# Kernel tuning notes

Measured on AMD Instinct MI355X. Metric: run time of the kernel, lower is better.

Reference implementation:

```python
import jax, jax.numpy as jnp
import numpy as np

B, H, S, D = 1, 8, 4096, 64
NSPAN, SPAN_LEN = 8, 512  # 8 contiguous spans of 512 tokens
RADIUS_SQ = 6.25          # default radius=2.5 squared (current_radius_sq buffer)


def setup_inputs() -> dict:
    key = jax.random.key(0)
    kq, kk, kv = jax.random.split(key, 3)
    q = jax.random.normal(kq, (B, H, S, D), jnp.float32)
    k = jax.random.normal(kk, (B, H, S, D), jnp.float32)
    v = jax.random.normal(kv, (B, H, S, D), jnp.float32)
    # span topology, as produced by update_buffers(spans)
    span_ids = jnp.repeat(jnp.arange(NSPAN, dtype=jnp.int32), SPAN_LEN)  # [S]
    causal_per_span = jnp.array([(i % 2) == 0 for i in range(NSPAN)])     # alternate causal/spatial
    is_causal = causal_per_span[span_ids]                                 # [S] bool
    # non-causal spans carry a 16x32 spatial grid (per _generate_grid); causal spans have coords 0
    gy, gx = jnp.meshgrid(jnp.arange(16, dtype=jnp.float32),
                          jnp.arange(32, dtype=jnp.float32), indexing='ij')
    grid = jnp.stack([gy, gx], axis=-1).reshape(SPAN_LEN, 2)
    coords = jnp.where(is_causal[:, None], 0.0, jnp.tile(grid, (NSPAN, 1)))  # [S,2]
    return {"q": q, "k": k, "v": v, "coords": coords,
            "span_ids": span_ids, "is_causal": is_causal}


def _mask(coords, span_ids, is_causal):
    # mask_mod from get_mask, vectorized over (q_idx, kv_idx) -> [S,S] bool
    qs = span_ids[:, None]
    ks = span_ids[None, :]
    is_history = qs > ks
    is_same = qs == ks
    idx = jnp.arange(span_ids.shape[0])
    valid_time = (~is_causal[:, None]) | (idx[:, None] >= idx[None, :])
    dist_sq = jnp.sum((coords[:, None, :] - coords[None, :, :]) ** 2, axis=-1)
    valid_space = dist_sq < RADIUS_SQ
    return is_history | (is_same & valid_time & valid_space)


def reference(q, k, v, coords, span_ids, is_causal):
    mask = _mask(coords, span_ids, is_causal)                       # [S,S]
    scale = 1.0 / jnp.sqrt(jnp.float32(D))
    scores = jnp.einsum('bhqd,bhkd->bhqk', q, k) * scale            # [B,H,S,S]
    scores = jnp.where(mask, scores, jnp.float32(-1e30))
    attn = jax.nn.softmax(scores, axis=-1)
    return jnp.einsum('bhqk,bhkd->bhqd', attn, v)                   # [B,H,S,D]
```

## Files before the change

### kernel.cpp

```cpp
#include <hip/hip_runtime.h>

#define S_LEN 4096
#define DH 64
#define SPAN 512
#define FIXED_M 8.0f

typedef _Float16 f16x8 __attribute__((ext_vector_type(8)));
typedef __fp16 fp16v2 __attribute__((ext_vector_type(2)));
typedef float f32x4 __attribute__((ext_vector_type(4)));

#define MFMA16 __builtin_amdgcn_mfma_f32_16x16x32_f16

__device__ __forceinline__ f16x8 load_cvt8(const float* __restrict__ p) {
  float4 a = *(const float4*)p;
  float4 b = *(const float4*)(p + 4);
  f16x8 r;
  r[0] = (_Float16)a.x; r[1] = (_Float16)a.y; r[2] = (_Float16)a.z; r[3] = (_Float16)a.w;
  r[4] = (_Float16)b.x; r[5] = (_Float16)b.y; r[6] = (_Float16)b.z; r[7] = (_Float16)b.w;
  return r;
}

__global__ __launch_bounds__(256) void prep_frag(const float* __restrict__ k,
                                                 const float* __restrict__ v,
                                                 _Float16* __restrict__ KF,
                                                 _Float16* __restrict__ VF) {
  const int b = blockIdx.x;
  const int h = b >> 7, tile = b & 127;
  const int kv0 = tile * 32;
  __shared__ _Float16 LK[32][64];
  __shared__ _Float16 LV[64][36];
  const int t = threadIdx.x;
  const int row = t >> 3, cb = (t & 7) * 8;
  {
    const float* kp = k + ((size_t)h * S_LEN + kv0 + row) * DH + cb;
    float4 a = *(const float4*)kp;
    float4 bq = *(const float4*)(kp + 4);
    LK[row][cb + 0] = (_Float16)a.x;  LK[row][cb + 1] = (_Float16)a.y;
    LK[row][cb + 2] = (_Float16)a.z;  LK[row][cb + 3] = (_Float16)a.w;
    LK[row][cb + 4] = (_Float16)bq.x; LK[row][cb + 5] = (_Float16)bq.y;
    LK[row][cb + 6] = (_Float16)bq.z; LK[row][cb + 7] = (_Float16)bq.w;
  }
  {
    const float* vp = v + ((size_t)h * S_LEN + kv0 + row) * DH + cb;
    float4 a = *(const float4*)vp;
    float4 bq = *(const float4*)(vp + 4);
    LV[cb + 0][row] = (_Float16)a.x;  LV[cb + 1][row] = (_Float16)a.y;
    LV[cb + 2][row] = (_Float16)a.z;  LV[cb + 3][row] = (_Float16)a.w;
    LV[cb + 4][row] = (_Float16)bq.x; LV[cb + 5][row] = (_Float16)bq.y;
    LV[cb + 6][row] = (_Float16)bq.z; LV[cb + 7][row] = (_Float16)bq.w;
  }
  __syncthreads();
  const int l = t & 63, c = l & 15, g = l >> 4;
  const size_t tb = (size_t)(h * 128 + tile) * 2048;
  {
    const int ch = t >> 6;
    f16x8 r = *(const f16x8*)&LK[16 * (ch >> 1) + c][32 * (ch & 1) + 8 * g];
    *(f16x8*)(KF + tb + (size_t)(ch * 64 + l) * 8) = r;
  }
  {
    const int dd = t >> 6;
    f16x8 r;
    #pragma unroll
    for (int jj = 0; jj < 4; ++jj) {
      r[jj]     = LV[16 * dd + c][4 * g + jj];
      r[4 + jj] = LV[16 * dd + c][16 + 4 * g + jj];
    }
    *(f16x8*)(VF + tb + (size_t)(dd * 64 + l) * 8) = r;
  }
}

template<int MODE>
__device__ __forceinline__ void kv_tile(
    const _Float16* __restrict__ kbase, const _Float16* __restrict__ vbase,
    int kt, int q_base, int c, int g,
    const f16x8 (&qf)[2][2], float (&l_run)[2], f32x4 (&of)[2][4])
{
  const int toff = (kt >> 5) * 2048;
  f16x8 kf0a = *(const f16x8*)(kbase + toff);
  f16x8 kf0b = *(const f16x8*)(kbase + toff + 512);
  f16x8 kf1a = *(const f16x8*)(kbase + toff + 1024);
  f16x8 kf1b = *(const f16x8*)(kbase + toff + 1536);
  f16x8 vf0  = *(const f16x8*)(vbase + toff);
  f16x8 vf1  = *(const f16x8*)(vbase + toff + 512);
  f16x8 vf2  = *(const f16x8*)(vbase + toff + 1024);
  f16x8 vf3  = *(const f16x8*)(vbase + toff + 1536);

  const float SCL = 0.18033688011112042f;

  #pragma unroll
  for (int grp = 0; grp < 2; ++grp) {
    f32x4 st0 = {0.f, 0.f, 0.f, 0.f};
    f32x4 st1 = {0.f, 0.f, 0.f, 0.f};
    st0 = MFMA16(kf0a, qf[grp][0], st0, 0, 0, 0);
    st0 = MFMA16(kf0b, qf[grp][1], st0, 0, 0, 0);
    st1 = MFMA16(kf1a, qf[grp][0], st1, 0, 0, 0);
    st1 = MFMA16(kf1b, qf[grp][1], st1, 0, 0, 0);

    const int qg = q_base + 16 * grp + c;
    float p[8];
    #pragma unroll
    for (int t = 0; t < 2; ++t) {
      #pragma unroll
      for (int r = 0; r < 4; ++r) {
        float pe = __builtin_amdgcn_exp2f(fmaf(t ? st1[r] : st0[r], SCL, -FIXED_M));
        if (MODE == 1) {
          int kvi = kt + 16 * t + 4 * g + r;
          pe = (kvi <= qg) ? pe : 0.f;
        } else if (MODE == 2) {
          int kvi = kt + 16 * t + 4 * g + r;
          int pq = qg & (SPAN - 1), pk = kvi & (SPAN - 1);
          int dy = (pq >> 5) - (pk >> 5);
          int dx = (pq & 31) - (pk & 31);
          pe = (dy * dy + dx * dx <= 6) ? pe : 0.f;
        }
        p[4 * t + r] = pe;
      }
    }
    l_run[grp] += ((p[0] + p[1]) + (p[2] + p[3])) + ((p[4] + p[5]) + (p[6] + p[7]));

    union { unsigned int w[4]; f16x8 v; } u;
    union { fp16v2 h; unsigned int w; } t0, t1, t2, t3;
    t0.h = __builtin_amdgcn_cvt_pkrtz(p[0], p[1]);
    t1.h = __builtin_amdgcn_cvt_pkrtz(p[2], p[3]);
    t2.h = __builtin_amdgcn_cvt_pkrtz(p[4], p[5]);
    t3.h = __builtin_amdgcn_cvt_pkrtz(p[6], p[7]);
    u.w[0] = t0.w; u.w[1] = t1.w; u.w[2] = t2.w; u.w[3] = t3.w;
    f16x8 pa = u.v;

    of[grp][0] = MFMA16(vf0, pa, of[grp][0], 0, 0, 0);
    of[grp][1] = MFMA16(vf1, pa, of[grp][1], 0, 0, 0);
    of[grp][2] = MFMA16(vf2, pa, of[grp][2], 0, 0, 0);
    of[grp][3] = MFMA16(vf3, pa, of[grp][3], 0, 0, 0);
  }
}

__global__ __launch_bounds__(256) void msa_attn13(
    const float* __restrict__ q, const _Float16* __restrict__ KF,
    const _Float16* __restrict__ VF, float* __restrict__ PO,
    float* __restrict__ PL)
{
  const int tid = threadIdx.x;
  const int lane = tid & 63, w = tid >> 6;
  const int c = lane & 15, g = lane >> 4;

  const int b = blockIdx.x;
  const int h = b & 7;
  const int unit = (b >> 3) * 4 + w;

  int s, sub, slot, klo, khi, mode;
  {
    int r = unit;
    if (r < 448) {
      s = 1;
      while (r >= 16 * s) { r -= 16 * s; ++s; }
      sub = r & 15;
      slot = r >> 4;
      klo = slot << 9;
      khi = klo + 512;
      mode = 0;
    } else {
      r -= 448;
      s = r >> 4; sub = r & 15;
      slot = s;
      const int hist_end = s * SPAN;
      const int q_base = s * SPAN + sub * 32;
      if ((s & 1) == 0) {
        klo = hist_end; khi = q_base + 32; mode = 1;
      } else {
        klo = q_base - 96; if (klo < hist_end) klo = hist_end;
        khi = q_base + 128;
        const int s1 = hist_end + SPAN; if (khi > s1) khi = s1;
        mode = 2;
      }
    }
  }
  const int q_base = s * SPAN + sub * 32;

  const float* Qh = q + (size_t)h * S_LEN * DH;
  const _Float16* kbase = KF + (size_t)h * 262144 + (size_t)lane * 8;
  const _Float16* vbase = VF + (size_t)h * 262144 + (size_t)lane * 8;

  f16x8 qf[2][2];
  #pragma unroll
  for (int grp = 0; grp < 2; ++grp) {
    const float* qp = Qh + (size_t)(q_base + 16 * grp + c) * DH + 8 * g;
    qf[grp][0] = load_cvt8(qp);
    qf[grp][1] = load_cvt8(qp + 32);
  }

  float l_run[2] = {0.f, 0.f};
  f32x4 of[2][4];
  #pragma unroll
  for (int a = 0; a < 2; ++a)
    #pragma unroll
    for (int bb = 0; bb < 4; ++bb) of[a][bb] = (f32x4){0.f, 0.f, 0.f, 0.f};

  if (mode == 0) {
    for (int kt = klo; kt < khi; kt += 32)
      kv_tile<0>(kbase, vbase, kt, q_base, c, g, qf, l_run, of);
  } else if (mode == 1) {
    for (int kt = klo; kt < khi; kt += 32)
      kv_tile<1>(kbase, vbase, kt, q_base, c, g, qf, l_run, of);
  } else {
    for (int kt = klo; kt < khi; kt += 32)
      kv_tile<2>(kbase, vbase, kt, q_base, c, g, qf, l_run, of);
  }

  #pragma unroll
  for (int grp = 0; grp < 2; ++grp) {
    l_run[grp] += __shfl_xor(l_run[grp], 16);
    l_run[grp] += __shfl_xor(l_run[grp], 32);
  }

  const size_t sl_idx = (size_t)(h * 128 + s * 16 + sub) * 8 + slot;
  float* po = PO + sl_idx * 2048;
  float* pl = PL + sl_idx * 32;
  if (g == 0) { pl[c] = l_run[0]; pl[16 + c] = l_run[1]; }
  #pragma unroll
  for (int grp = 0; grp < 2; ++grp)
    #pragma unroll
    for (int dd = 0; dd < 4; ++dd)
      *(f32x4*)(po + (16 * grp + c) * 64 + 16 * dd + 4 * g) = of[grp][dd];
}

__global__ __launch_bounds__(256) void finalize13(const float* __restrict__ PO,
                                                  const float* __restrict__ PL,
                                                  float* __restrict__ out) {
  const int strip = blockIdx.x;
  const int h = strip >> 7, idx = strip & 127;
  const int s = idx >> 4, sub = idx & 15;
  const int t = threadIdx.x;
  const int row = t >> 3, colb = (t & 7) * 8;
  const float* po = PO + (size_t)strip * 8 * 2048 + row * 64 + colb;
  const float* pl = PL + (size_t)strip * 8 * 32 + row;
  f32x4 a0 = {0.f, 0.f, 0.f, 0.f}, a1 = {0.f, 0.f, 0.f, 0.f};
  float l = 0.f;
  for (int sl = 0; sl <= s; ++sl) {
    a0 += *(const f32x4*)(po + sl * 2048);
    a1 += *(const f32x4*)(po + sl * 2048 + 4);
    l  += pl[sl * 32];
  }
  const float inv = 1.0f / l;
  f32x4 o0, o1;
  #pragma unroll
  for (int j = 0; j < 4; ++j) { o0[j] = a0[j] * inv; o1[j] = a1[j] * inv; }
  const int orow = s * SPAN + sub * 32 + row;
  float* op = out + ((size_t)h * S_LEN + orow) * DH + colb;
  *(f32x4*)op = o0;
  *(f32x4*)(op + 4) = o1;
}

__global__ __launch_bounds__(256, 3) void msa_attn10(
    const float* __restrict__ q, const _Float16* __restrict__ KF,
    const _Float16* __restrict__ VF, float* __restrict__ out)
{
  const int tid = threadIdx.x;
  const int lane = tid & 63, w = tid >> 6;
  const int c = lane & 15, g = lane >> 4;

  const int i = blockIdx.x;
  const int h = i & 7;
  const int m = i >> 3;
  const int jj = m >> 5;
  const int sidx = ((m & 7) + jj) & 7;
  const int span = (sidx & 1) ? 7 - (sidx >> 1) : (sidx >> 1);
  const int sub = ((m >> 3) & 3) * 4 + jj;
  const int q_base = span * SPAN + sub * 32;

  const float* Qh = q + (size_t)h * S_LEN * DH;
  const _Float16* kbase = KF + (size_t)h * 262144 + (size_t)lane * 8;
  const _Float16* vbase = VF + (size_t)h * 262144 + (size_t)lane * 8;
  float* Oh = out + (size_t)h * S_LEN * DH;

  f16x8 qf[2][2];
  #pragma unroll
  for (int grp = 0; grp < 2; ++grp) {
    const float* qp = Qh + (size_t)(q_base + 16 * grp + c) * DH + 8 * g;
    qf[grp][0] = load_cvt8(qp);
    qf[grp][1] = load_cvt8(qp + 32);
  }

  float l_run[2] = {0.f, 0.f};
  f32x4 of[2][4];
  #pragma unroll
  for (int a = 0; a < 2; ++a)
    #pragma unroll
    for (int bb = 0; bb < 4; ++bb) of[a][bb] = (f32x4){0.f, 0.f, 0.f, 0.f};

  const int hist_end = span * SPAN;
  for (int kt = 32 * w; kt < hist_end; kt += 128)
    kv_tile<0>(kbase, vbase, kt, q_base, c, g, qf, l_run, of);

  if ((span & 1) == 0) {
    for (int kt = hist_end + 32 * w; kt < q_base + 32; kt += 128)
      kv_tile<1>(kbase, vbase, kt, q_base, c, g, qf, l_run, of);
  } else {
    int klo = q_base - 96;
    if (klo < hist_end) klo = hist_end;
    int khi = q_base + 128;
    const int s1 = hist_end + SPAN;
    if (khi > s1) khi = s1;
    for (int kt = klo + 32 * w; kt < khi; kt += 128)
      kv_tile<2>(kbase, vbase, kt, q_base, c, g, qf, l_run, of);
  }

  #pragma unroll
  for (int grp = 0; grp < 2; ++grp) {
    l_run[grp] += __shfl_xor(l_run[grp], 16);
    l_run[grp] += __shfl_xor(l_run[grp], 32);
  }

  __shared__ float sl[4][2][16];
  __shared__ float sof[4][2][4][16][17];
  if (g == 0) { sl[w][0][c] = l_run[0]; sl[w][1][c] = l_run[1]; }
  #pragma unroll
  for (int grp = 0; grp < 2; ++grp)
    #pragma unroll
    for (int dd = 0; dd < 4; ++dd)
      #pragma unroll
      for (int r = 0; r < 4; ++r)
        sof[w][grp][dd][4 * g + r][c] = of[grp][dd][r];
  __syncthreads();

  const int mc = tid & 15, mgrp = (tid >> 4) & 1, mdd = (tid >> 5) & 3;
  const int mhalf = tid >> 7;
  float ls = sl[0][mgrp][mc] + sl[1][mgrp][mc] + sl[2][mgrp][mc] + sl[3][mgrp][mc];
  float inv = 1.0f / ls;
  const int row = q_base + 16 * mgrp + mc;
  #pragma unroll
  for (int dbi = 0; dbi < 2; ++dbi) {
    const int db = 2 * mhalf + dbi;
    f32x4 o4;
    #pragma unroll
    for (int j = 0; j < 4; ++j) {
      int dc = db * 4 + j;
      o4[j] = (sof[0][mgrp][mdd][dc][mc] + sof[1][mgrp][mdd][dc][mc]
             + sof[2][mgrp][mdd][dc][mc] + sof[3][mgrp][mdd][dc][mc]) * inv;
    }
    *(f32x4*)(Oh + (size_t)row * DH + mdd * 16 + db * 4) = o4;
  }
}

template<int MODE>
__device__ __forceinline__ void kv_tile_fb(
    const float* __restrict__ Kh, const float* __restrict__ Vh,
    int kt, int qg_row, int c, int g,
    const f16x8 (&qf)[2], float& m_run, float& l_run, f32x4 (&of)[4])
{
  f16x8 kf0a = load_cvt8(Kh + (kt +      c) * DH + 8 * g);
  f16x8 kf0b = load_cvt8(Kh + (kt +      c) * DH + 8 * g + 32);
  f16x8 kf1a = load_cvt8(Kh + (kt + 16 + c) * DH + 8 * g);
  f16x8 kf1b = load_cvt8(Kh + (kt + 16 + c) * DH + 8 * g + 32);

  f32x4 st0 = {0.f, 0.f, 0.f, 0.f};
  f32x4 st1 = {0.f, 0.f, 0.f, 0.f};
  st0 = MFMA16(kf0a, qf[0], st0, 0, 0, 0);
  st0 = MFMA16(kf0b, qf[1], st0, 0, 0, 0);
  st1 = MFMA16(kf1a, qf[0], st1, 0, 0, 0);
  st1 = MFMA16(kf1b, qf[1], st1, 0, 0, 0);

  const float SCL = 0.18033688011112042f;
  float ss[8];
  #pragma unroll
  for (int t = 0; t < 2; ++t) {
    #pragma unroll
    for (int r = 0; r < 4; ++r) {
      float vsc = (t ? st1[r] : st0[r]) * SCL;
      if (MODE == 1) {
        int kv = kt + 16 * t + 4 * g + r;
        vsc = (kv <= qg_row) ? vsc : -1e30f;
      } else if (MODE == 2) {
        int kv = kt + 16 * t + 4 * g + r;
        int pq = qg_row & (SPAN - 1), pk = kv & (SPAN - 1);
        int dy = (pq >> 5) - (pk >> 5);
        int dx = (pq & 31) - (pk & 31);
        vsc = (dy * dy + dx * dx <= 6) ? vsc : -1e30f;
      }
      ss[t * 4 + r] = vsc;
    }
  }

  float pmax = ss[0];
  #pragma unroll
  for (int j = 1; j < 8; ++j) pmax = fmaxf(pmax, ss[j]);
  pmax = fmaxf(pmax, __shfl_xor(pmax, 16));
  pmax = fmaxf(pmax, __shfl_xor(pmax, 32));

  float m_new = fmaxf(m_run, pmax);
  float fac = exp2f(m_run - m_new);
  m_run = m_new;

  float p[8];
  float psum = 0.f;
  #pragma unroll
  for (int j = 0; j < 8; ++j) { p[j] = exp2f(ss[j] - m_new); psum += p[j]; }
  psum += __shfl_xor(psum, 16);
  psum += __shfl_xor(psum, 32);
  l_run = l_run * fac + psum;

  float fr0 = __shfl(fac, 4 * g + 0);
  float fr1 = __shfl(fac, 4 * g + 1);
  float fr2 = __shfl(fac, 4 * g + 2);
  float fr3 = __shfl(fac, 4 * g + 3);
  #pragma unroll
  for (int cc = 0; cc < 4; ++cc) {
    of[cc][0] *= fr0; of[cc][1] *= fr1; of[cc][2] *= fr2; of[cc][3] *= fr3;
  }

  f16x8 pa;
  #pragma unroll
  for (int j = 0; j < 8; ++j) pa[j] = (_Float16)p[j];

  #pragma unroll
  for (int cc = 0; cc < 4; ++cc) {
    f16x8 vb;
    #pragma unroll
    for (int j = 0; j < 8; ++j) {
      int kv = kt + ((j < 4) ? (4 * g + j) : (16 + 4 * g + (j - 4)));
      vb[j] = (_Float16)Vh[(size_t)kv * DH + 16 * cc + c];
    }
    of[cc] = MFMA16(pa, vb, of[cc], 0, 0, 0);
  }
}

__global__ __launch_bounds__(64) void msa_attn(
    const float* __restrict__ q, const float* __restrict__ k,
    const float* __restrict__ v, float* __restrict__ out)
{
  const int lane = threadIdx.x;
  const int c = lane & 15, g = lane >> 4;

  const int i = blockIdx.x;
  const int h = i & 7;
  const int grp = (i >> 3) & 31;
  const int t3 = i >> 8;
  const int span = (t3 + grp) & 7;
  const int q_base = span * SPAN + grp * 16;

  const float* Qh = q + (size_t)h * S_LEN * DH;
  const float* Kh = k + (size_t)h * S_LEN * DH;
  const float* Vh = v + (size_t)h * S_LEN * DH;
  float* Oh = out + (size_t)h * S_LEN * DH;

  f16x8 qf[2];
  qf[0] = load_cvt8(Qh + (size_t)(q_base + c) * DH + 8 * g);
  qf[1] = load_cvt8(Qh + (size_t)(q_base + c) * DH + 8 * g + 32);

  float m_run = -1e30f, l_run = 0.f;
  f32x4 of[4] = {{0,0,0,0},{0,0,0,0},{0,0,0,0},{0,0,0,0}};
  const int qg_row = q_base + c;

  const int hist_end = span * SPAN;
  for (int kt = 0; kt < hist_end; kt += 32)
    kv_tile_fb<0>(Kh, Vh, kt, qg_row, c, g, qf, m_run, l_run, of);

  const int s0 = hist_end;
  if ((span & 1) == 0) {
    const int khi = (q_base + 16 + 31) & ~31;
    for (int kt = s0; kt < khi; kt += 32)
      kv_tile_fb<1>(Kh, Vh, kt, qg_row, c, g, qf, m_run, l_run, of);
  } else {
    int klo = (q_base - 66) & ~31;
    if (klo < s0) klo = s0;
    int khi = (q_base + 81 + 32) & ~31;
    const int s1 = s0 + SPAN;
    if (khi > s1) khi = s1;
    for (int kt = klo; kt < khi; kt += 32)
      kv_tile_fb<2>(Kh, Vh, kt, qg_row, c, g, qf, m_run, l_run, of);
  }

  #pragma unroll
  for (int r = 0; r < 4; ++r) {
    float inv = 1.0f / __shfl(l_run, 4 * g + r);
    int row = q_base + 4 * g + r;
    #pragma unroll
    for (int cc = 0; cc < 4; ++cc)
      Oh[(size_t)row * DH + 16 * cc + c] = of[cc][r] * inv;
  }
}

extern "C" void kernel_launch(void* const* d_in, const int* in_sizes, int n_in,
                              void* d_out, int out_size, void* d_ws, size_t ws_size,
                              hipStream_t stream) {
  const float* q = (const float*)d_in[0];
  const float* k = (const float*)d_in[1];
  const float* v = (const float*)d_in[2];
  float* out = (float*)d_out;

  const size_t elems = (size_t)8 * S_LEN * DH;
  const size_t kv_bytes = elems * 2 * 2;
  const size_t po_bytes = (size_t)1024 * 8 * 2048 * 4;
  const size_t pl_bytes = (size_t)1024 * 8 * 32 * 4;
  if (ws_size >= kv_bytes + po_bytes + pl_bytes) {
    _Float16* KF = (_Float16*)d_ws;
    _Float16* VF = KF + elems;
    float* PO = (float*)((char*)d_ws + kv_bytes);
    float* PL = (float*)((char*)d_ws + kv_bytes + po_bytes);
    prep_frag<<<dim3(1024), dim3(256), 0, stream>>>(k, v, KF, VF);
    msa_attn13<<<dim3(1152), dim3(256), 0, stream>>>(q, KF, VF, PO, PL);
    finalize13<<<dim3(1024), dim3(256), 0, stream>>>(PO, PL, out);
  } else if (ws_size >= kv_bytes) {
    _Float16* KF = (_Float16*)d_ws;
    _Float16* VF = KF + elems;
    prep_frag<<<dim3(1024), dim3(256), 0, stream>>>(k, v, KF, VF);
    msa_attn10<<<dim3(1024), dim3(256), 0, stream>>>(q, KF, VF, out);
  } else {
    msa_attn<<<dim3(2048), dim3(64), 0, stream>>>(q, k, v, out);
  }
}
```

Baseline: 54.65 us.

## Share K/V tiles across block's waves via double-buffered LDS staging

Work units are regrouped so the four waves of a block handle four adjacent 32-row query strips against the same K/V range, rather than four independent units. Each 32-key K/V tile is loaded once per block into a double-buffered shared-memory buffer, with the next tile prefetched into registers during compute. This aims to cut redundant global/L2 traffic by sharing tiles across waves. In exchange it adds a block barrier per tile, LDS reads, and some waves in causal/spatial spans now scan wider key ranges than they need, doing extra masked work.

```diff
diff --git a/kernel.cpp b/kernel.cpp
--- a/kernel.cpp
+++ b/kernel.cpp
@@ -70,20 +70,21 @@
 }
 
 template<int MODE>
-__device__ __forceinline__ void kv_tile(
-    const _Float16* __restrict__ kbase, const _Float16* __restrict__ vbase,
-    int kt, int q_base, int c, int g,
+__device__ __forceinline__ void tile_lds(
+    const _Float16* kb, const _Float16* vb,
+    int kt, int q_base, int c, int g, int lane,
     const f16x8 (&qf)[2][2], float (&l_run)[2], f32x4 (&of)[2][4])
 {
-  const int toff = (kt >> 5) * 2048;
-  f16x8 kf0a = *(const f16x8*)(kbase + toff);
-  f16x8 kf0b = *(const f16x8*)(kbase + toff + 512);
-  f16x8 kf1a = *(const f16x8*)(kbase + toff + 1024);
-  f16x8 kf1b = *(const f16x8*)(kbase + toff + 1536);
-  f16x8 vf0  = *(const f16x8*)(vbase + toff);
-  f16x8 vf1  = *(const f16x8*)(vbase + toff + 512);
-  f16x8 vf2  = *(const f16x8*)(vbase + toff + 1024);
-  f16x8 vf3  = *(const f16x8*)(vbase + toff + 1536);
+  const _Float16* kp = kb + lane * 8;
+  f16x8 kf0a = *(const f16x8*)(kp);
+  f16x8 kf0b = *(const f16x8*)(kp + 512);
+  f16x8 kf1a = *(const f16x8*)(kp + 1024);
+  f16x8 kf1b = *(const f16x8*)(kp + 1536);
+  const _Float16* vp = vb + lane * 8;
+  f16x8 vf0  = *(const f16x8*)(vp);
+  f16x8 vf1  = *(const f16x8*)(vp + 512);
+  f16x8 vf2  = *(const f16x8*)(vp + 1024);
+  f16x8 vf3  = *(const f16x8*)(vp + 1536);
 
   const float SCL = 0.18033688011112042f;
 
@@ -134,7 +135,7 @@
   }
 }
 
-__global__ __launch_bounds__(256) void msa_attn13(
+__global__ __launch_bounds__(256) void msa_attn15(
     const float* __restrict__ q, const _Float16* __restrict__ KF,
     const _Float16* __restrict__ VF, float* __restrict__ PO,
     float* __restrict__ PL)
@@ -145,40 +146,39 @@
 
   const int b = blockIdx.x;
   const int h = b & 7;
-  const int unit = (b >> 3) * 4 + w;
-
-  int s, sub, slot, klo, khi, mode;
-  {
-    int r = unit;
-    if (r < 448) {
-      s = 1;
-      while (r >= 16 * s) { r -= 16 * s; ++s; }
-      sub = r & 15;
-      slot = r >> 4;
-      klo = slot << 9;
-      khi = klo + 512;
-      mode = 0;
+  int r = b >> 3;
+
+  int s, quad, slot, klo, khi, mode;
+  if (r < 112) {
+    s = 1;
+    while (r >= 4 * s) { r -= 4 * s; ++s; }
+    quad = r & 3; slot = r >> 2;
+    klo = slot << 9; khi = klo + 512;
+    mode = 0;
+  } else {
+    r -= 112;
+    s = r >> 2; quad = r & 3;
+    slot = s;
+    const int he = s * SPAN;
+    const int qb0 = he + quad * 128;
+    if ((s & 1) == 0) {
+      klo = he; khi = qb0 + 128; mode = 1;
     } else {
-      r -= 448;
-      s = r >> 4; sub = r & 15;
-      slot = s;
-      const int hist_end = s * SPAN;
-      const int q_base = s * SPAN + sub * 32;
-      if ((s & 1) == 0) {
-        klo = hist_end; khi = q_base + 32; mode = 1;
-      } else {
-        klo = q_base - 96; if (klo < hist_end) klo = hist_end;
-        khi = q_base + 128;
-        const int s1 = hist_end + SPAN; if (khi > s1) khi = s1;
-        mode = 2;
-      }
-    }
-  }
+      klo = qb0 - 96; if (klo < he) klo = he;
+      khi = qb0 + 256;
+      const int s1 = he + SPAN; if (khi > s1) khi = s1;
+      mode = 2;
+    }
+  }
+  const int sub = quad * 4 + w;
   const int q_base = s * SPAN + sub * 32;
 
   const float* Qh = q + (size_t)h * S_LEN * DH;
-  const _Float16* kbase = KF + (size_t)h * 262144 + (size_t)lane * 8;
-  const _Float16* vbase = VF + (size_t)h * 262144 + (size_t)lane * 8;
+  const _Float16* KFh = KF + (size_t)h * 262144;
+  const _Float16* VFh = VF + (size_t)h * 262144;
+
+  __shared__ _Float16 KBUF[2][2048];
+  __shared__ _Float16 VBUF[2][2048];
 
   f16x8 qf[2][2];
   #pragma unroll
@@ -195,15 +195,35 @@
     #pragma unroll
     for (int bb = 0; bb < 4; ++bb) of[a][bb] = (f32x4){0.f, 0.f, 0.f, 0.f};
 
-  if (mode == 0) {
-    for (int kt = klo; kt < khi; kt += 32)
-      kv_tile<0>(kbase, vbase, kt, q_base, c, g, qf, l_run, of);
-  } else if (mode == 1) {
-    for (int kt = klo; kt < khi; kt += 32)
-      kv_tile<1>(kbase, vbase, kt, q_base, c, g, qf, l_run, of);
-  } else {
-    for (int kt = klo; kt < khi; kt += 32)
-      kv_tile<2>(kbase, vbase, kt, q_base, c, g, qf, l_run, of);
+  {
+    const int toff = (klo >> 5) * 2048 + tid * 8;
+    f16x8 kr = *(const f16x8*)(KFh + toff);
+    f16x8 vr = *(const f16x8*)(VFh + toff);
+    *(f16x8*)&KBUF[0][tid * 8] = kr;
+    *(f16x8*)&VBUF[0][tid * 8] = vr;
+  }
+  __syncthreads();
+
+  int cur = 0;
+  for (int kt = klo; kt < khi; kt += 32) {
+    const bool more = (kt + 32 < khi);
+    f16x8 kr, vr;
+    if (more) {
+      const int toff = ((kt + 32) >> 5) * 2048 + tid * 8;
+      kr = *(const f16x8*)(KFh + toff);
+      vr = *(const f16x8*)(VFh + toff);
+    }
+
+    if (mode == 0)      tile_lds<0>(KBUF[cur], VBUF[cur], kt, q_base, c, g, lane, qf, l_run, of);
+    else if (mode == 1) tile_lds<1>(KBUF[cur], VBUF[cur], kt, q_base, c, g, lane, qf, l_run, of);
+    else                tile_lds<2>(KBUF[cur], VBUF[cur], kt, q_base, c, g, lane, qf, l_run, of);
+
+    if (more) {
+      *(f16x8*)&KBUF[cur ^ 1][tid * 8] = kr;
+      *(f16x8*)&VBUF[cur ^ 1][tid * 8] = vr;
+    }
+    __syncthreads();
+    cur ^= 1;
   }
 
   #pragma unroll
@@ -250,6 +270,71 @@
   *(f32x4*)(op + 4) = o1;
 }
 
+template<int MODE>
+__device__ __forceinline__ void kv_tile(
+    const _Float16* __restrict__ kbase, const _Float16* __restrict__ vbase,
+    int kt, int q_base, int c, int g,
+    const f16x8 (&qf)[2][2], float (&l_run)[2], f32x4 (&of)[2][4])
+{
+  const int toff = (kt >> 5) * 2048;
+  f16x8 kf0a = *(const f16x8*)(kbase + toff);
+  f16x8 kf0b = *(const f16x8*)(kbase + toff + 512);
+  f16x8 kf1a = *(const f16x8*)(kbase + toff + 1024);
+  f16x8 kf1b = *(const f16x8*)(kbase + toff + 1536);
+  f16x8 vf0  = *(const f16x8*)(vbase + toff);
+  f16x8 vf1  = *(const f16x8*)(vbase + toff + 512);
+  f16x8 vf2  = *(const f16x8*)(vbase + toff + 1024);
+  f16x8 vf3  = *(const f16x8*)(vbase + toff + 1536);
+
+  const float SCL = 0.18033688011112042f;
+
+  #pragma unroll
+  for (int grp = 0; grp < 2; ++grp) {
+    f32x4 st0 = {0.f, 0.f, 0.f, 0.f};
+    f32x4 st1 = {0.f, 0.f, 0.f, 0.f};
+    st0 = MFMA16(kf0a, qf[grp][0], st0, 0, 0, 0);
+    st0 = MFMA16(kf0b, qf[grp][1], st0, 0, 0, 0);
+    st1 = MFMA16(kf1a, qf[grp][0], st1, 0, 0, 0);
+    st1 = MFMA16(kf1b, qf[grp][1], st1, 0, 0, 0);
+
+    const int qg = q_base + 16 * grp + c;
+    float p[8];
+    #pragma unroll
+    for (int t = 0; t < 2; ++t) {
+      #pragma unroll
+      for (int r = 0; r < 4; ++r) {
+        float pe = __builtin_amdgcn_exp2f(fmaf(t ? st1[r] : st0[r], SCL, -FIXED_M));
+        if (MODE == 1) {
+          int kvi = kt + 16 * t + 4 * g + r;
+          pe = (kvi <= qg) ? pe : 0.f;
+        } else if (MODE == 2) {
+          int kvi = kt + 16 * t + 4 * g + r;
+          int pq = qg & (SPAN - 1), pk = kvi & (SPAN - 1);
+          int dy = (pq >> 5) - (pk >> 5);
+          int dx = (pq & 31) - (pk & 31);
+          pe = (dy * dy + dx * dx <= 6) ? pe : 0.f;
+        }
+        p[4 * t + r] = pe;
+      }
+    }
+    l_run[grp] += ((p[0] + p[1]) + (p[2] + p[3])) + ((p[4] + p[5]) + (p[6] + p[7]));
+
+    union { unsigned int w[4]; f16x8 v; } u;
+    union { fp16v2 h; unsigned int w; } t0, t1, t2, t3;
+    t0.h = __builtin_amdgcn_cvt_pkrtz(p[0], p[1]);
+    t1.h = __builtin_amdgcn_cvt_pkrtz(p[2], p[3]);
+    t2.h = __builtin_amdgcn_cvt_pkrtz(p[4], p[5]);
+    t3.h = __builtin_amdgcn_cvt_pkrtz(p[6], p[7]);
+    u.w[0] = t0.w; u.w[1] = t1.w; u.w[2] = t2.w; u.w[3] = t3.w;
+    f16x8 pa = u.v;
+
+    of[grp][0] = MFMA16(vf0, pa, of[grp][0], 0, 0, 0);
+    of[grp][1] = MFMA16(vf1, pa, of[grp][1], 0, 0, 0);
+    of[grp][2] = MFMA16(vf2, pa, of[grp][2], 0, 0, 0);
+    of[grp][3] = MFMA16(vf3, pa, of[grp][3], 0, 0, 0);
+  }
+}
+
 __global__ __launch_bounds__(256, 3) void msa_attn10(
     const float* __restrict__ q, const _Float16* __restrict__ KF,
     const _Float16* __restrict__ VF, float* __restrict__ out)
@@ -497,7 +582,7 @@
     float* PO = (float*)((char*)d_ws + kv_bytes);
     float* PL = (float*)((char*)d_ws + kv_bytes + po_bytes);
     prep_frag<<<dim3(1024), dim3(256), 0, stream>>>(k, v, KF, VF);
-    msa_attn13<<<dim3(1152), dim3(256), 0, stream>>>(q, KF, VF, PO, PL);
+    msa_attn15<<<dim3(1152), dim3(256), 0, stream>>>(q, KF, VF, PO, PL);
     finalize13<<<dim3(1024), dim3(256), 0, stream>>>(PO, PL, out);
   } else if (ws_size >= kv_bytes) {
     _Float16* KF = (_Float16*)d_ws;
```

Result: slower. 62.79 us (+14.9%).
